# Kernel tuning notes

Hardware: AMD Instinct MI355X
Metric: run time of the kernel (lower is better)

Reference implementation:

```python
import jax, jax.numpy as jnp
import numpy as np
import math

B, S, E_PHI, E_F, H_F, N_HEADS = 2, 2048, 1024, 1024, 1024, 16


def setup_inputs() -> dict:
    key = jax.random.key(0)
    ks = jax.random.split(key, 7)
    return {
        "q": jax.random.normal(ks[0], (B, S, E_PHI), dtype=jnp.float32),
        "k": jax.random.normal(ks[1], (B, S, E_PHI), dtype=jnp.float32),
        "v": jax.random.normal(ks[2], (B, S, E_F), dtype=jnp.float32),
        # weights stored as [in, out]; applied as x @ W (same math as nn.Linear with W^T)
        "W_q": jax.random.normal(ks[3], (E_PHI, H_F), dtype=jnp.float32) * 0.02,
        "W_k": jax.random.normal(ks[4], (E_PHI, H_F), dtype=jnp.float32) * 0.02,
        "W_v": jax.random.normal(ks[5], (E_F, H_F), dtype=jnp.float32) * 0.02,
        "W_o": jax.random.normal(ks[6], (H_F, E_F), dtype=jnp.float32) * 0.02,
    }


def reference(q, k, v, W_q, W_k, W_v, W_o):
    Bq, Sq, _ = q.shape
    Dh = H_F // N_HEADS
    scale = 1.0 / math.sqrt(H_F)
    # projections -> [B, H, S, Dh]
    qh = (q @ W_q).reshape(Bq, Sq, N_HEADS, Dh).transpose(0, 2, 1, 3)
    kh = (k @ W_k).reshape(Bq, Sq, N_HEADS, Dh).transpose(0, 2, 1, 3)
    vh = (v @ W_v).reshape(Bq, Sq, N_HEADS, Dh).transpose(0, 2, 1, 3)
    # near-causal mask: mask out j >= i (triu incl. diagonal), EXCEPT position [0,0]
    mask = jnp.triu(jnp.ones((Sq, Sq), dtype=bool), 0).at[0, 0].set(False)
    scores = jnp.einsum('bhsd,bhtd->bhst', qh, kh) * scale  # [B,H,S,S]
    scores = jnp.where(mask, -jnp.inf, scores)
    probs = jax.nn.softmax(scores, axis=-1)  # dropout = identity (eval mode)
    out = jnp.einsum('bhst,bhtd->bhsd', probs, vh)  # [B,H,S,Dh]
    out = out.transpose(0, 2, 1, 3).reshape(Bq, Sq, H_F)
    return out @ W_o
```

## Files before the change

### kernel.cpp

```cpp
#include <hip/hip_runtime.h>
#include <type_traits>

#define S_LEN 2048
#define NHEAD 16
#define DHEAD 64
#define EMB   1024
#define NBATCH 2

typedef __bf16 bf16_t;
typedef bf16_t bf16x8 __attribute__((ext_vector_type(8)));
typedef float  f32x4  __attribute__((ext_vector_type(4)));
typedef unsigned short us_t;
typedef us_t   us8    __attribute__((ext_vector_type(8)));
typedef us_t   us4    __attribute__((ext_vector_type(4)));
typedef unsigned int u32x4 __attribute__((ext_vector_type(4)));
typedef unsigned int u32x2 __attribute__((ext_vector_type(2)));
typedef short  s16x4  __attribute__((ext_vector_type(4)));

static __device__ __forceinline__ bf16x8 ld_bf16x8(const us_t* p) {
  return __builtin_bit_cast(bf16x8, *reinterpret_cast<const us8*>(p));
}
static __device__ __forceinline__ us_t f2bf(float f) {
  bf16_t h = (bf16_t)f;
  return __builtin_bit_cast(us_t, h);
}
static __device__ __forceinline__ unsigned cvt_pk_bf16(float lo, float hi) {
  unsigned r;
  asm("v_cvt_pk_bf16_f32 %0, %1, %2" : "=v"(r) : "v"(lo), "v"(hi));
  return r;
}
#if __has_builtin(__builtin_amdgcn_exp2f)
#define EXP2(x) __builtin_amdgcn_exp2f(x)
#else
#define EXP2(x) exp2f(x)
#endif
static __device__ __forceinline__ void gload16(const void* g, void* lds) {
  __builtin_amdgcn_global_load_lds((const __attribute__((address_space(1))) void*)g,
                                   (__attribute__((address_space(3))) void*)lds,
                                   16, 0, 0);
}

__global__ __launch_bounds__(256) void prep(const float* __restrict__ q,
                                            const float* __restrict__ k,
                                            const float* __restrict__ v,
                                            const float* __restrict__ W0,
                                            const float* __restrict__ W1,
                                            const float* __restrict__ W2,
                                            const float* __restrict__ W3,
                                            us_t* __restrict__ Qb,
                                            us_t* __restrict__ Kb,
                                            us_t* __restrict__ Vb,
                                            us_t* __restrict__ T0,
                                            us_t* __restrict__ T1,
                                            us_t* __restrict__ T2,
                                            us_t* __restrict__ T3) {
  const int z = blockIdx.z;
  if (z < 3) {
    const float* A = (z == 0) ? q : (z == 1) ? k : v;
    us_t* O = (z == 0) ? Qb : (z == 1) ? Kb : Vb;
    const int flat = blockIdx.y * 32 + blockIdx.x;
    const size_t i = ((size_t)flat * 256 + threadIdx.x) * 8;
    f32x4 lo = *reinterpret_cast<const f32x4*>(A + i);
    f32x4 hi = *reinterpret_cast<const f32x4*>(A + i + 4);
    us8 w;
#pragma unroll
    for (int j = 0; j < 4; ++j) { w[j] = f2bf(lo[j]); w[j + 4] = f2bf(hi[j]); }
    *reinterpret_cast<us8*>(O + i) = w;
  } else {
    if (blockIdx.y >= EMB / 32) return;
    __shared__ float tile[32][33];
    const int zz = z - 3;
    const float* W = (zz == 0) ? W0 : (zz == 1) ? W1 : (zz == 2) ? W2 : W3;
    us_t* WT = (zz == 0) ? T0 : (zz == 1) ? T1 : (zz == 2) ? T2 : T3;
    const int n0 = blockIdx.x * 32, k0 = blockIdx.y * 32;
    const int tx = threadIdx.x & 31, ty = threadIdx.x >> 5;
#pragma unroll
    for (int i = 0; i < 32; i += 8)
      tile[ty + i][tx] = W[(size_t)(k0 + ty + i) * EMB + n0 + tx];
    __syncthreads();
#pragma unroll
    for (int i = 0; i < 32; i += 8)
      WT[(size_t)(n0 + ty + i) * EMB + k0 + tx] = f2bf(tile[tx][ty + i]);
  }
}

template<int MODE>
static __device__ __forceinline__ void gemm_core(const us_t* __restrict__ A,
                                                 const us_t* __restrict__ BT,
                                                 void* __restrict__ O,
                                                 int mt, int nt,
                                                 char (*As)[8192], char (*Bs)[8192]) {
  const int lane = threadIdx.x & 63;
  const int wave = threadIdx.x >> 6;
  const int wm = (wave >> 1) * 64;
  const int wn = (wave & 1) * 64;
  const int lr = lane & 15;
  const int lg = lane >> 4;

  f32x4 acc[4][4] = {};

  auto stage = [&](int buf, int k0) {
#pragma unroll
    for (int i = 0; i < 2; ++i) {
      const int seg = wave * 2 + i;
      const int r = seg * 16 + (lane >> 2);
      const int cb = (lane & 3) * 16;
      gload16((const char*)A + ((size_t)(mt * 128 + r) * EMB + k0) * 2 + cb,
              &As[buf][seg * 1024]);
      gload16((const char*)BT + ((size_t)(nt * 128 + r) * EMB + k0) * 2 + cb,
              &Bs[buf][seg * 1024]);
    }
  };

  stage(0, 0);
  __syncthreads();

  for (int ks = 0; ks < EMB / 32; ++ks) {
    const int cur = ks & 1;
    if (ks + 1 < EMB / 32) stage(cur ^ 1, (ks + 1) * 32);
    bf16x8 af[4], bfr[4];
#pragma unroll
    for (int i = 0; i < 4; ++i)
      af[i] = ld_bf16x8((const us_t*)&As[cur][(wm + 16 * i + lr) * 64 + lg * 16]);
#pragma unroll
    for (int j = 0; j < 4; ++j)
      bfr[j] = ld_bf16x8((const us_t*)&Bs[cur][(wn + 16 * j + lr) * 64 + lg * 16]);
#pragma unroll
    for (int i = 0; i < 4; ++i)
#pragma unroll
      for (int j = 0; j < 4; ++j)
        acc[i][j] = __builtin_amdgcn_mfma_f32_16x16x32_bf16(af[i], bfr[j], acc[i][j], 0, 0, 0);
    __syncthreads();
  }

  const int crow = (lane >> 4) * 4;
#pragma unroll
  for (int i = 0; i < 4; ++i)
#pragma unroll
    for (int j = 0; j < 4; ++j)
#pragma unroll
      for (int r = 0; r < 4; ++r) {
        const int m = mt * 128 + wm + 16 * i + crow + r;
        const int n = nt * 128 + wn + 16 * j + lr;
        const float val = acc[i][j][r];
        if constexpr (MODE == 2) {
          ((float*)O)[(size_t)m * EMB + n] = val;
        } else {
          us_t* o = (us_t*)O;
          const int b = m >> 11, s = m & (S_LEN - 1);
          const int h = n >> 6, d = n & 63;
          if constexpr (MODE == 0)
            o[(((size_t)(b * NHEAD + h) * S_LEN + s) << 6) + d] = f2bf(val);
          else
            o[((size_t)(b * NHEAD + h) * DHEAD + d) * S_LEN + s] = f2bf(val);
        }
      }
}

__global__ __launch_bounds__(256) void proj3(const us_t* __restrict__ A0,
                                             const us_t* __restrict__ A1,
                                             const us_t* __restrict__ A2,
                                             const us_t* __restrict__ B0,
                                             const us_t* __restrict__ B1,
                                             const us_t* __restrict__ B2,
                                             us_t* __restrict__ O0,
                                             us_t* __restrict__ O1,
                                             us_t* __restrict__ O2) {
  __shared__ char As[2][8192];
  __shared__ char Bs[2][8192];
  const int f = blockIdx.x;
  const int w = (f & 7) * 96 + (f >> 3);
  const int z = w >> 8;
  const int rem = w & 255;
  const int mt = rem >> 3, nt = rem & 7;
  const us_t* A = (z == 0) ? A0 : (z == 1) ? A1 : A2;
  const us_t* BT = (z == 0) ? B0 : (z == 1) ? B1 : B2;
  us_t* O = (z == 0) ? O0 : (z == 1) ? O1 : O2;
  if (z < 2)
    gemm_core<0>(A, BT, O, mt, nt, As, Bs);
  else
    gemm_core<1>(A, BT, O, mt, nt, As, Bs);
}

__global__ __launch_bounds__(256) void gemmout(const us_t* __restrict__ A,
                                               const us_t* __restrict__ BT,
                                               float* __restrict__ O) {
  __shared__ char As[2][8192];
  __shared__ char Bs[2][8192];
  const int f = blockIdx.x;
  const int w = (f & 7) * 32 + (f >> 3);
  const int mt = w >> 3, nt = w & 7;
  gemm_core<2>(A, BT, O, mt, nt, As, Bs);
}

__global__ __launch_bounds__(256, 4) void attn64(const us_t* __restrict__ Qh,
                                                 const us_t* __restrict__ Kh,
                                                 const us_t* __restrict__ Vt,
                                                 us_t* __restrict__ AO) {
  __shared__ char Ks[2][8192];
  __shared__ char Vs[2][8192];
  const int flat = blockIdx.y * 32 + blockIdx.x;
  const int bh = (flat & 7) * 4 + ((flat >> 3) & 3);
  const int qt = 31 - (flat >> 5);
  const int lane = threadIdx.x & 63;
  const int wave = threadIdx.x >> 6;
  const int lr = lane & 15;
  const int lg = lane >> 4;
  const int q_glob = qt * 64 + wave * 16 + lr;

  const us_t* qbase = Qh + ((size_t)bh * S_LEN + q_glob) * DHEAD;
  bf16x8 qf[2] = { ld_bf16x8(qbase + lg * 8), ld_bf16x8(qbase + 32 + lg * 8) };

  const us_t* kbase0 = Kh + (size_t)bh * S_LEN * DHEAD;
  const us_t* vbase0 = Vt + (size_t)bh * DHEAD * S_LEN;

  int koff[8];
#pragma unroll
  for (int ks = 0; ks < 2; ++ks)
#pragma unroll
    for (int j = 0; j < 4; ++j)
      koff[ks * 4 + j] = (16 * j + lr) * 128 + ((ks * 64 + lg * 16) ^ ((lr & 7) << 4));
  int voff[16];
#pragma unroll
  for (int jk = 0; jk < 4; ++jk)
#pragma unroll
    for (int jd = 0; jd < 4; ++jd)
      voff[jk * 4 + jd] = (16 * jd + lr) * 128 + ((32 * jk + 8 * lg) ^ ((lr & 7) << 4));

  auto stage = [&](int buf, int t0) {
#pragma unroll
    for (int i = 0; i < 2; ++i) {
      const int seg = wave * 2 + i;
      const int r = seg * 8 + (lane >> 3);
      const int c16 = (lane & 7) ^ (lane >> 3);
      gload16(kbase0 + (size_t)(t0 + r) * DHEAD + c16 * 8, &Ks[buf][seg * 1024]);
      gload16(vbase0 + (size_t)r * S_LEN + t0 + c16 * 8, &Vs[buf][seg * 1024]);
    }
  };

  f32x4 oaccT[4] = {};
  float mrow = -1e9f;
  float lsum = 0.f;
  const float c = 0.045084220f;

  stage(0, 0);
  __syncthreads();

  for (int tt = 0; tt <= qt; ++tt) {
    const int cur = tt & 1;
    if (tt < qt) stage(cur ^ 1, (tt + 1) * 64);

    f32x4 sc[4] = {};
    __builtin_amdgcn_s_setprio(1);
#pragma unroll
    for (int ks = 0; ks < 2; ++ks)
#pragma unroll
      for (int j = 0; j < 4; ++j) {
        bf16x8 ak = ld_bf16x8((const us_t*)&Ks[cur][koff[ks * 4 + j]]);
        sc[j] = __builtin_amdgcn_mfma_f32_16x16x32_bf16(ak, qf[ks], sc[j], 0, 0, 0);
      }
    __builtin_amdgcn_s_setprio(0);

    if (tt == qt) {
#pragma unroll
      for (int j = 0; j < 4; ++j)
#pragma unroll
        for (int r = 0; r < 4; ++r) {
          const int t_g = tt * 64 + 16 * j + 4 * lg + r;
          if (!((t_g < q_glob) || (q_glob == 0 && t_g == 0))) sc[j][r] = -1e30f;
        }
    }

    float mx = sc[0][0];
#pragma unroll
    for (int j = 0; j < 4; ++j)
#pragma unroll
      for (int r = 0; r < 4; ++r) mx = fmaxf(mx, sc[j][r]);
    const float mxc = mx * c;
    if (__any(mxc > mrow + 8.f)) {
      float mc = mxc;
      mc = fmaxf(mc, __shfl_xor(mc, 16, 64));
      mc = fmaxf(mc, __shfl_xor(mc, 32, 64));
      const float m2 = fmaxf(mrow, mc);
      const float alpha = EXP2(mrow - m2);
      lsum *= alpha;
#pragma unroll
      for (int j = 0; j < 4; ++j)
#pragma unroll
        for (int r = 0; r < 4; ++r) oaccT[j][r] *= alpha;
      mrow = m2;
    }

    unsigned int pk[4][2];
    float ps = 0.f;
#pragma unroll
    for (int j = 0; j < 4; ++j) {
      float p0 = EXP2(__builtin_fmaf(sc[j][0], c, -mrow));
      float p1 = EXP2(__builtin_fmaf(sc[j][1], c, -mrow));
      float p2 = EXP2(__builtin_fmaf(sc[j][2], c, -mrow));
      float p3 = EXP2(__builtin_fmaf(sc[j][3], c, -mrow));
      ps += (p0 + p1) + (p2 + p3);
      pk[j][0] = cvt_pk_bf16(p0, p1);
      pk[j][1] = cvt_pk_bf16(p2, p3);
    }
    lsum += ps;

    __builtin_amdgcn_s_setprio(1);
#pragma unroll
    for (int jk = 0; jk < 4; ++jk) {
      s16x4 pf = __builtin_bit_cast(s16x4, (u32x2){pk[jk][0], pk[jk][1]});
#pragma unroll
      for (int jd = 0; jd < 4; ++jd) {
        s16x4 av = __builtin_bit_cast(s16x4,
            *reinterpret_cast<const us4*>(&Vs[cur][voff[jk * 4 + jd]]));
        oaccT[jd] = __builtin_amdgcn_mfma_f32_16x16x16bf16_1k(av, pf, oaccT[jd], 0, 0, 0);
      }
    }
    __builtin_amdgcn_s_setprio(0);
    __syncthreads();
  }

  lsum += __shfl_xor(lsum, 16, 64);
  lsum += __shfl_xor(lsum, 32, 64);
  const float inv = 1.0f / lsum;
  const int b = bh >> 4, h = bh & 15;
  us_t* aout = AO + (size_t)(b * S_LEN + q_glob) * EMB + h * DHEAD;
#pragma unroll
  for (int j = 0; j < 4; ++j) {
    us4 w;
#pragma unroll
    for (int r = 0; r < 4; ++r) w[r] = f2bf(oaccT[j][r] * inv);
    *reinterpret_cast<us4*>(aout + 16 * j + 4 * lg) = w;
  }
}

extern "C" void kernel_launch(void* const* d_in, const int* in_sizes, int n_in,
                              void* d_out, int out_size, void* d_ws, size_t ws_size,
                              hipStream_t stream) {
  const float* q  = (const float*)d_in[0];
  const float* k  = (const float*)d_in[1];
  const float* v  = (const float*)d_in[2];
  const float* Wq = (const float*)d_in[3];
  const float* Wk = (const float*)d_in[4];
  const float* Wv = (const float*)d_in[5];
  const float* Wo = (const float*)d_in[6];
  float* out = (float*)d_out;

  char* ws = (char*)d_ws;
  const size_t MB = 1024 * 1024;
  us_t* WqT = (us_t*)(ws + 0 * MB);
  us_t* WkT = (us_t*)(ws + 2 * MB);
  us_t* WvT = (us_t*)(ws + 4 * MB);
  us_t* WoT = (us_t*)(ws + 6 * MB);
  us_t* Qh  = (us_t*)(ws + 8 * MB);
  us_t* Kh  = (us_t*)(ws + 16 * MB);
  us_t* Vt  = (us_t*)(ws + 24 * MB);
  us_t* AO  = (us_t*)(ws + 32 * MB);
  us_t* Qb  = (us_t*)(ws + 32 * MB);
  us_t* Kb  = (us_t*)(ws + 40 * MB);
  us_t* Vb  = (us_t*)(ws + 48 * MB);

  prep<<<dim3(32, 64, 7), 256, 0, stream>>>(q, k, v, Wq, Wk, Wv, Wo,
                                            Qb, Kb, Vb, WqT, WkT, WvT, WoT);

  proj3<<<768, 256, 0, stream>>>(Qb, Kb, Vb, WqT, WkT, WvT, Qh, Kh, Vt);

  attn64<<<dim3(S_LEN / 64, NBATCH * NHEAD), 256, 0, stream>>>(Qh, Kh, Vt, AO);

  gemmout<<<256, 256, 0, stream>>>(AO, WoT, out);
}
```

Before: 130.6 us.

## Triple-buffer GEMM loads, vectorize stores, reorder attention tile schedule

The GEMM core moves from double to triple buffering in LDS: loads run two stages ahead and use explicit vmcnt waits with raw barriers instead of a __syncthreads per step. The transposed V output is written as 4-wide vector stores, and the prep cast uses packed bf16 conversion. Attention query tiles are dispatched in a zig-zag order so that heavy and light causal tiles are mixed in each wave of blocks. Together these aim to hide global-load latency and reduce store and load-imbalance overhead. The larger LDS footprint may reduce GEMM occupancy.

```diff
diff --git a/kernel.cpp b/kernel.cpp
--- a/kernel.cpp
+++ b/kernel.cpp
@@ -62,10 +62,9 @@
     const size_t i = ((size_t)flat * 256 + threadIdx.x) * 8;
     f32x4 lo = *reinterpret_cast<const f32x4*>(A + i);
     f32x4 hi = *reinterpret_cast<const f32x4*>(A + i + 4);
-    us8 w;
-#pragma unroll
-    for (int j = 0; j < 4; ++j) { w[j] = f2bf(lo[j]); w[j + 4] = f2bf(hi[j]); }
-    *reinterpret_cast<us8*>(O + i) = w;
+    u32x4 w = { cvt_pk_bf16(lo[0], lo[1]), cvt_pk_bf16(lo[2], lo[3]),
+                cvt_pk_bf16(hi[0], hi[1]), cvt_pk_bf16(hi[2], hi[3]) };
+    *reinterpret_cast<u32x4*>(O + i) = w;
   } else {
     if (blockIdx.y >= EMB / 32) return;
     __shared__ float tile[32][33];
@@ -96,6 +95,7 @@
   const int wn = (wave & 1) * 64;
   const int lr = lane & 15;
   const int lg = lane >> 4;
+  constexpr int NK = EMB / 32;
 
   f32x4 acc[4][4] = {};
 
@@ -111,50 +111,69 @@
               &Bs[buf][seg * 1024]);
     }
   };
-
-  stage(0, 0);
-  __syncthreads();
-
-  for (int ks = 0; ks < EMB / 32; ++ks) {
-    const int cur = ks & 1;
-    if (ks + 1 < EMB / 32) stage(cur ^ 1, (ks + 1) * 32);
+  auto mfma_step = [&](int buf) {
     bf16x8 af[4], bfr[4];
 #pragma unroll
     for (int i = 0; i < 4; ++i)
-      af[i] = ld_bf16x8((const us_t*)&As[cur][(wm + 16 * i + lr) * 64 + lg * 16]);
+      af[i] = ld_bf16x8((const us_t*)&As[buf][(wm + 16 * i + lr) * 64 + lg * 16]);
 #pragma unroll
     for (int j = 0; j < 4; ++j)
-      bfr[j] = ld_bf16x8((const us_t*)&Bs[cur][(wn + 16 * j + lr) * 64 + lg * 16]);
+      bfr[j] = ld_bf16x8((const us_t*)&Bs[buf][(wn + 16 * j + lr) * 64 + lg * 16]);
 #pragma unroll
     for (int i = 0; i < 4; ++i)
 #pragma unroll
       for (int j = 0; j < 4; ++j)
         acc[i][j] = __builtin_amdgcn_mfma_f32_16x16x32_bf16(af[i], bfr[j], acc[i][j], 0, 0, 0);
-    __syncthreads();
+  };
+
+  stage(0, 0);
+  stage(1, 32);
+  asm volatile("s_waitcnt vmcnt(4)" ::: "memory");
+  __builtin_amdgcn_s_barrier();
+
+  for (int ks = 0; ks < NK; ++ks) {
+    const int cur = ks % 3;
+    if (ks + 2 < NK) stage((ks + 2) % 3, (ks + 2) * 32);
+    mfma_step(cur);
+    if (ks + 1 < NK) {
+      if (ks + 2 < NK) asm volatile("s_waitcnt vmcnt(4)" ::: "memory");
+      else             asm volatile("s_waitcnt vmcnt(0)" ::: "memory");
+      __builtin_amdgcn_s_barrier();
+    }
   }
 
   const int crow = (lane >> 4) * 4;
 #pragma unroll
   for (int i = 0; i < 4; ++i)
 #pragma unroll
-    for (int j = 0; j < 4; ++j)
-#pragma unroll
-      for (int r = 0; r < 4; ++r) {
-        const int m = mt * 128 + wm + 16 * i + crow + r;
+    for (int j = 0; j < 4; ++j) {
+      if constexpr (MODE == 1) {
+        const int m = mt * 128 + wm + 16 * i + crow;
         const int n = nt * 128 + wn + 16 * j + lr;
-        const float val = acc[i][j][r];
-        if constexpr (MODE == 2) {
-          ((float*)O)[(size_t)m * EMB + n] = val;
-        } else {
-          us_t* o = (us_t*)O;
-          const int b = m >> 11, s = m & (S_LEN - 1);
-          const int h = n >> 6, d = n & 63;
-          if constexpr (MODE == 0)
+        const int b = m >> 11, s = m & (S_LEN - 1);
+        const int h = n >> 6, d = n & 63;
+        us4 w;
+#pragma unroll
+        for (int r = 0; r < 4; ++r) w[r] = f2bf(acc[i][j][r]);
+        *reinterpret_cast<us4*>((us_t*)O +
+            ((size_t)(b * NHEAD + h) * DHEAD + d) * S_LEN + s) = w;
+      } else {
+#pragma unroll
+        for (int r = 0; r < 4; ++r) {
+          const int m = mt * 128 + wm + 16 * i + crow + r;
+          const int n = nt * 128 + wn + 16 * j + lr;
+          const float val = acc[i][j][r];
+          if constexpr (MODE == 2) {
+            ((float*)O)[(size_t)m * EMB + n] = val;
+          } else {
+            us_t* o = (us_t*)O;
+            const int b = m >> 11, s = m & (S_LEN - 1);
+            const int h = n >> 6, d = n & 63;
             o[(((size_t)(b * NHEAD + h) * S_LEN + s) << 6) + d] = f2bf(val);
-          else
-            o[((size_t)(b * NHEAD + h) * DHEAD + d) * S_LEN + s] = f2bf(val);
+          }
         }
       }
+    }
 }
 
 __global__ __launch_bounds__(256) void proj3(const us_t* __restrict__ A0,
@@ -166,8 +185,8 @@
                                              us_t* __restrict__ O0,
                                              us_t* __restrict__ O1,
                                              us_t* __restrict__ O2) {
-  __shared__ char As[2][8192];
-  __shared__ char Bs[2][8192];
+  __shared__ char As[3][8192];
+  __shared__ char Bs[3][8192];
   const int f = blockIdx.x;
   const int w = (f & 7) * 96 + (f >> 3);
   const int z = w >> 8;
@@ -185,8 +204,8 @@
 __global__ __launch_bounds__(256) void gemmout(const us_t* __restrict__ A,
                                                const us_t* __restrict__ BT,
                                                float* __restrict__ O) {
-  __shared__ char As[2][8192];
-  __shared__ char Bs[2][8192];
+  __shared__ char As[3][8192];
+  __shared__ char Bs[3][8192];
   const int f = blockIdx.x;
   const int w = (f & 7) * 32 + (f >> 3);
   const int mt = w >> 3, nt = w & 7;
@@ -201,7 +220,9 @@
   __shared__ char Vs[2][8192];
   const int flat = blockIdx.y * 32 + blockIdx.x;
   const int bh = (flat & 7) * 4 + ((flat >> 3) & 3);
-  const int qt = 31 - (flat >> 5);
+  const int g = flat >> 5;
+  const int Q = g >> 3, p = g & 7;
+  const int qt = (Q == 0) ? 31 - p : (Q == 1) ? 16 + p : (Q == 2) ? 15 - p : p;
   const int lane = threadIdx.x & 63;
   const int wave = threadIdx.x >> 6;
   const int lr = lane & 15;
@@ -365,7 +386,7 @@
 
   proj3<<<768, 256, 0, stream>>>(Qb, Kb, Vb, WqT, WkT, WvT, Qh, Kh, Vt);
 
-  attn64<<<dim3(S_LEN / 64, NBATCH * NHEAD), 256, 0, stream>>>(Qh, Kh, Vt, AO);
+  attn64<<<dim3(32, 32), 256, 0, stream>>>(Qh, Kh, Vt, AO);
 
   gemmout<<<256, 256, 0, stream>>>(AO, WoT, out);
 }
```

After: 127.5 us. 1.02x faster.
